# Kernel optimization log

Measured on AMD Instinct MI355X. Metric: run time of the kernel, lower is better.

Reference implementation:

```python
import jax, jax.numpy as jnp
import numpy as np

D_MODEL = 1024
NUM_HEADS = 16
DEPTH = D_MODEL // NUM_HEADS
B, S = 4, 2048


def setup_inputs() -> dict:
    key = jax.random.key(0)
    ks = jax.random.split(key, 11)
    sc = 1.0 / np.sqrt(D_MODEL)
    return {
        "query": jax.random.normal(ks[0], (B, S, D_MODEL), jnp.float32),
        "key_": jax.random.normal(ks[1], (B, S, D_MODEL), jnp.float32),
        "value": jax.random.normal(ks[2], (B, S, D_MODEL), jnp.float32),
        # torch Linear: y = x @ W.T + b, W shape [out, in]
        "Wq": jax.random.normal(ks[3], (D_MODEL, D_MODEL), jnp.float32) * sc,
        "bq": jax.random.normal(ks[4], (D_MODEL,), jnp.float32) * sc,
        "Wk": jax.random.normal(ks[5], (D_MODEL, D_MODEL), jnp.float32) * sc,
        "bk": jax.random.normal(ks[6], (D_MODEL,), jnp.float32) * sc,
        "Wv": jax.random.normal(ks[7], (D_MODEL, D_MODEL), jnp.float32) * sc,
        "bv": jax.random.normal(ks[8], (D_MODEL,), jnp.float32) * sc,
        "Wo": jax.random.normal(ks[9], (D_MODEL, D_MODEL), jnp.float32) * sc,
        "bo": jax.random.normal(ks[10], (D_MODEL,), jnp.float32) * sc,
    }


def _split_heads(x):
    # [B,S,D] -> [B,H,S,depth]
    b, s, _ = x.shape
    return x.reshape(b, s, NUM_HEADS, DEPTH).transpose(0, 2, 1, 3)


def reference(query, key_, value, Wq, bq, Wk, bk, Wv, bv, Wo, bo):
    Q = _split_heads(query @ Wq.T + bq)
    K = _split_heads(key_ @ Wk.T + bk)
    V = _split_heads(value @ Wv.T + bv)
    scale = 1.0 / jnp.sqrt(jnp.float32(DEPTH))
    scores = jnp.einsum("bhqd,bhkd->bhqk", Q, K) * scale  # [B,H,S,S]
    attention_weights = jax.nn.softmax(scores, axis=-1)
    out = jnp.einsum("bhqk,bhkd->bhqd", attention_weights, V)
    out = out.transpose(0, 2, 1, 3).reshape(query.shape[0], -1, D_MODEL)
    out = out @ Wo.T + bo
    return out, attention_weights
```

## Files before the change

kernel.cpp:

```cpp
#include <hip/hip_runtime.h>

#define NHEAD 16
#define SEQ 2048
#define DMODEL 1024
#define BB 4
#define MROWS (BB*SEQ)
#define NBH (BB*NHEAD)
#define NT (SEQ/32)

typedef float f32x4 __attribute__((ext_vector_type(4)));
typedef _Float16 f16x8 __attribute__((ext_vector_type(8)));
typedef _Float16 f16x4 __attribute__((ext_vector_type(4)));

static __device__ __forceinline__ f32x4 mfma16(f16x8 a, f16x8 b, f32x4 c) {
  return __builtin_amdgcn_mfma_f32_16x16x32_f16(a, b, c, 0, 0, 0);
}

static __device__ __forceinline__ void split2(float x, unsigned short& hi, unsigned short& lo) {
  _Float16 h = (_Float16)x;
  hi = __builtin_bit_cast(unsigned short, h);
  lo = __builtin_bit_cast(unsigned short, (_Float16)(x - (float)h));
}

static __device__ __forceinline__ void gload_lds16(const unsigned short* g, unsigned short* l) {
  __builtin_amdgcn_global_load_lds(
      (const __attribute__((address_space(1))) unsigned int*)g,
      (__attribute__((address_space(3))) unsigned int*)l, 16, 0, 0);
}

__global__ __launch_bounds__(256)
void round_f16(const float* __restrict__ src, unsigned short* __restrict__ dst, int n4)
{
  int i = blockIdx.x*256 + threadIdx.x;
  const int stride = gridDim.x*256;
  for (; i < n4; i += stride) {
    const float4 x = ((const float4*)src)[i];
    ushort4 h;
    h.x = __builtin_bit_cast(unsigned short, (_Float16)x.x);
    h.y = __builtin_bit_cast(unsigned short, (_Float16)x.y);
    h.z = __builtin_bit_cast(unsigned short, (_Float16)x.z);
    h.w = __builtin_bit_cast(unsigned short, (_Float16)x.w);
    ((ushort4*)dst)[i] = h;
  }
}

__global__ __launch_bounds__(256)
void split_f32(const float* __restrict__ src, unsigned short* __restrict__ hi,
               unsigned short* __restrict__ lo, int n4)
{
  int i = blockIdx.x*256 + threadIdx.x;
  const int stride = gridDim.x*256;
  for (; i < n4; i += stride) {
    const float4 x = ((const float4*)src)[i];
    ushort4 h, l;
    split2(x.x, h.x, l.x); split2(x.y, h.y, l.y);
    split2(x.z, h.z, l.z); split2(x.w, h.w, l.w);
    ((ushort4*)hi)[i] = h;
    ((ushort4*)lo)[i] = l;
  }
}

static __device__ __forceinline__ void stage_proj(
    unsigned short* ab, unsigned short* bb,
    const unsigned short* __restrict__ Xf,
    const unsigned short* __restrict__ Wh, const unsigned short* __restrict__ Wl,
    int m0, int n0, int k0, int tid)
{
#pragma unroll
  for (int r = 0; r < 2; ++r) {
    const int gi = r*256 + tid;
    const int row = gi >> 2, c = gi & 3;
    const int lg = c ^ ((row >> 1) & 3);
    gload_lds16(Xf + (size_t)(m0+row)*DMODEL + k0 + lg*8,
                ab + r*2048 + (tid & 0xC0)*8);
  }
#pragma unroll
  for (int r = 0; r < 4; ++r) {
    const int gi = r*256 + tid;
    const int row = gi >> 3, c = gi & 7;
    const int sg = c ^ (row & 7);
    const unsigned short* src = (sg < 4)
        ? (Wh + (size_t)(n0+row)*DMODEL + k0 + sg*8)
        : (Wl + (size_t)(n0+row)*DMODEL + k0 + (sg-4)*8);
    gload_lds16(src, bb + r*2048 + (tid & 0xC0)*8);
  }
}

template<int MODE>
__global__ __launch_bounds__(256, 3)
void proj_gemm(const unsigned short* __restrict__ Xf,
               const unsigned short* __restrict__ Wh, const unsigned short* __restrict__ Wl,
               const float* __restrict__ bias, float oscale,
               unsigned short* __restrict__ o16, float* __restrict__ o_f32)
{
  __shared__ unsigned short As[2][128][32];
  __shared__ unsigned short Bs[2][128][64];
  const int tid  = threadIdx.x;
  const int wid  = tid >> 6, lane = tid & 63;
  const int g    = lane >> 4, r16 = lane & 15;
  const int id   = blockIdx.y*64 + blockIdx.x;
  const int xcd  = id & 7, slot = id >> 3;
  const int m0   = (xcd*8 + (slot & 7)) * 128;
  const int n0   = (slot >> 3) * 128;
  const int wr   = wid >> 1, wc = wid & 1;

  f32x4 acc[4][4] = {};

  stage_proj(&As[0][0][0], &Bs[0][0][0], Xf, Wh, Wl, m0, n0, 0, tid);
  asm volatile("s_waitcnt vmcnt(0)" ::: "memory");
  __builtin_amdgcn_s_barrier();

  for (int kt = 0; kt < 32; ++kt) {
    const int cur = kt & 1;
    if (kt < 31)
      stage_proj(&As[cur^1][0][0], &Bs[cur^1][0][0], Xf, Wh, Wl, m0, n0, (kt+1)*32, tid);

    const unsigned short (*Asb)[32] = As[cur];
    const unsigned short (*Bsb)[64] = Bs[cur];
    f16x8 a[4], b_h[4], b_l[4];
#pragma unroll
    for (int t = 0; t < 4; ++t) {
      const int ar = wr*64 + t*16 + r16;
      a[t] = *(const f16x8*)((const char*)&Asb[ar][0] + ((g ^ ((ar >> 1) & 3)) << 4));
      const int br = wc*64 + t*16 + r16;
      const char* pb = (const char*)&Bsb[br][0];
      b_h[t] = *(const f16x8*)(pb + (((g    ) ^ (br & 7)) << 4));
      b_l[t] = *(const f16x8*)(pb + (((4 | g) ^ (br & 7)) << 4));
    }
    __builtin_amdgcn_s_setprio(1);
#pragma unroll
    for (int mt = 0; mt < 4; ++mt)
#pragma unroll
      for (int nt = 0; nt < 4; ++nt) {
        acc[mt][nt] = mfma16(a[mt], b_h[nt], acc[mt][nt]);
        acc[mt][nt] = mfma16(a[mt], b_l[nt], acc[mt][nt]);
      }
    __builtin_amdgcn_s_setprio(0);

    if (kt < 31) {
      asm volatile("s_waitcnt vmcnt(0)" ::: "memory");
      __builtin_amdgcn_s_barrier();
    }
  }

#pragma unroll
  for (int nt = 0; nt < 4; ++nt) {
    const int n  = n0 + wc*64 + nt*16 + r16;
    const float bn = bias[n];
#pragma unroll
    for (int mt = 0; mt < 4; ++mt) {
      const int mb = m0 + wr*64 + mt*16 + g*4;
      if (MODE == 0) {
#pragma unroll
        for (int j = 0; j < 4; ++j) {
          const int m = mb + j;
          const int bt = m >> 11, s = m & (SEQ-1);
          const int hh = n >> 6,  d = n & 63;
          o16[(((size_t)(bt*NHEAD + hh)*SEQ + s) << 6) + d] =
              __builtin_bit_cast(unsigned short, (_Float16)((acc[mt][nt][j] + bn) * oscale));
        }
      } else if (MODE == 1) {
        const int bt = mb >> 11, sb = mb & (SEQ-1);
        const int hh = n >> 6,  d = n & 63;
        ushort4 v;
        v.x = __builtin_bit_cast(unsigned short, (_Float16)(acc[mt][nt][0] + bn));
        v.y = __builtin_bit_cast(unsigned short, (_Float16)(acc[mt][nt][1] + bn));
        v.z = __builtin_bit_cast(unsigned short, (_Float16)(acc[mt][nt][2] + bn));
        v.w = __builtin_bit_cast(unsigned short, (_Float16)(acc[mt][nt][3] + bn));
        *(ushort4*)(o16 + ((size_t)(bt*NHEAD + hh)*64 + d)*SEQ + sb) = v;
      } else {
#pragma unroll
        for (int j = 0; j < 4; ++j)
          o_f32[(size_t)(mb + j)*DMODEL + n] = acc[mt][nt][j] + bn;
      }
    }
  }
}

static __device__ __forceinline__ void stage_k(unsigned short* dst,
    const unsigned short* __restrict__ Kf, size_t kbase, int k0, int tid)
{
  const int row = tid >> 3, c = tid & 7;
  const int sg = c ^ (row & 7);
  gload_lds16(Kf + kbase + (size_t)(k0+row)*64 + sg*8, dst + (tid & 0xC0)*8);
}

static __device__ __forceinline__ void stage_v(unsigned short* dst,
    const unsigned short* __restrict__ Vtg, int bh, int k0, int tid)
{
  const int row = tid >> 2, c = tid & 3;
  const int lg = c ^ ((row >> 1) & 3);
  gload_lds16(Vtg + ((size_t)bh*64 + row)*SEQ + k0 + lg*8, dst + (tid & 0xC0)*8);
}

__global__ __launch_bounds__(256, 4)
void attn_fused(const unsigned short* __restrict__ Qf, const unsigned short* __restrict__ Kf,
                const unsigned short* __restrict__ Vtg,
                float* __restrict__ wout, unsigned short* __restrict__ of16)
{
  __shared__ unsigned short Ks[4][32][64];
  __shared__ unsigned short Vs[4][64][32];
  __shared__ unsigned short PA[4][16][40];
  const int tid = threadIdx.x, wid = tid >> 6, lane = tid & 63;
  const int g = lane >> 4, r16 = lane & 15;
  const int id = blockIdx.y*32 + blockIdx.x;
  const int xcd = id & 7, slot = id >> 3;
  const int bh = (slot >> 5)*8 + xcd;
  const int bx = slot & 31;
  const int bt = bh >> 4, hh = bh & (NHEAD-1);
  const int s0 = bx*64 + wid*16;
  const size_t kbase = (size_t)bh*SEQ*64;

  const size_t qoff = ((size_t)bh*SEQ + s0 + r16)*64 + (size_t)g*8;
  const f16x8 qh0 = *(const f16x8*)(Qf + qoff);
  const f16x8 qh1 = *(const f16x8*)(Qf + qoff + 32);

  float lp = 0.f;
  stage_k(&Ks[0][0][0], Kf, kbase, 0, tid);
  stage_k(&Ks[1][0][0], Kf, kbase, 32, tid);
  asm volatile("s_waitcnt vmcnt(1)" ::: "memory");
  __builtin_amdgcn_s_barrier();
  for (int kt = 0; kt < NT; ++kt) {
    const int cur = kt & 3;
    const bool pf = kt < NT-2;
    if (pf) stage_k(&Ks[(kt+2)&3][0][0], Kf, kbase, (kt+2)*32, tid);
#pragma unroll
    for (int sub = 0; sub < 2; ++sub) {
      const int krow = sub*16 + r16;
      const char* pk = (const char*)&Ks[cur][krow][0];
      const int sx = krow & 7;
      const f16x8 kh0 = *(const f16x8*)(pk + (((g    ) ^ sx) << 4));
      const f16x8 kh1 = *(const f16x8*)(pk + (((4 | g) ^ sx) << 4));
      f32x4 acc = {};
      __builtin_amdgcn_s_setprio(1);
      acc = mfma16(kh0, qh0, acc);
      acc = mfma16(kh1, qh1, acc);
      __builtin_amdgcn_s_setprio(0);
#pragma unroll
      for (int j = 0; j < 4; ++j) lp += __builtin_exp2f(acc[j]);
    }
    if (pf) { asm volatile("s_waitcnt vmcnt(1)" ::: "memory"); }
    else    { asm volatile("s_waitcnt vmcnt(0)" ::: "memory"); }
    __builtin_amdgcn_s_barrier();
  }
  lp += __shfl_xor(lp, 16);
  lp += __shfl_xor(lp, 32);
  const float li = 1.0f / lp;

  f32x4 acco[4] = {};
  char* paw = (char*)&PA[wid][0][0];

  stage_k(&Ks[0][0][0], Kf, kbase, 0, tid);
  stage_v(&Vs[0][0][0], Vtg, bh, 0, tid);
  stage_k(&Ks[1][0][0], Kf, kbase, 32, tid);
  stage_v(&Vs[1][0][0], Vtg, bh, 32, tid);
  asm volatile("s_waitcnt vmcnt(2)" ::: "memory");
  __builtin_amdgcn_s_barrier();
  for (int kt = 0; kt < NT; ++kt) {
    const int cur = kt & 3;
    if (kt < NT-2) {
      stage_k(&Ks[(kt+2)&3][0][0], Kf, kbase, (kt+2)*32, tid);
      stage_v(&Vs[(kt+2)&3][0][0], Vtg, bh, (kt+2)*32, tid);
    }
#pragma unroll
    for (int sub = 0; sub < 2; ++sub) {
      const int krow = sub*16 + r16;
      const char* pk = (const char*)&Ks[cur][krow][0];
      const int sx = krow & 7;
      const f16x8 kh0 = *(const f16x8*)(pk + (((g    ) ^ sx) << 4));
      const f16x8 kh1 = *(const f16x8*)(pk + (((4 | g) ^ sx) << 4));
      f32x4 acc = {};
      __builtin_amdgcn_s_setprio(1);
      acc = mfma16(kh0, qh0, acc);
      acc = mfma16(kh1, qh1, acc);
      __builtin_amdgcn_s_setprio(0);
      f32x4 w4;
      f16x4 p4;
#pragma unroll
      for (int j = 0; j < 4; ++j) {
        w4[j] = __builtin_exp2f(acc[j]) * li;
        p4[j] = (_Float16)w4[j];
      }
      float* wp = wout + ((size_t)bh*SEQ + s0 + r16)*SEQ + kt*32 + sub*16 + 4*g;
      __builtin_nontemporal_store(w4, (f32x4*)wp);
      *(f16x4*)(paw + r16*80 + ((((2*sub + (g >> 1)) ^ (r16 & 3)) << 4) | ((g & 1) << 3))) = p4;
    }
    asm volatile("s_waitcnt lgkmcnt(0)" ::: "memory");
    const f16x8 pa = *(const f16x8*)(paw + r16*80 + ((g ^ (r16 & 3)) << 4));
    __builtin_amdgcn_s_setprio(1);
#pragma unroll
    for (int nt = 0; nt < 4; ++nt) {
      const int vrow = nt*16 + r16;
      const f16x8 vv = *(const f16x8*)((const char*)&Vs[cur][vrow][0] +
                                       ((g ^ ((vrow >> 1) & 3)) << 4));
      acco[nt] = mfma16(pa, vv, acco[nt]);
    }
    __builtin_amdgcn_s_setprio(0);
    if (kt == 0) {
      asm volatile("s_waitcnt vmcnt(4)" ::: "memory"); __builtin_amdgcn_s_barrier();
    } else if (kt < NT-2) {
      asm volatile("s_waitcnt vmcnt(6)" ::: "memory"); __builtin_amdgcn_s_barrier();
    } else if (kt == NT-2) {
      asm volatile("s_waitcnt vmcnt(4)" ::: "memory"); __builtin_amdgcn_s_barrier();
    }
  }

#pragma unroll
  for (int nt = 0; nt < 4; ++nt)
#pragma unroll
    for (int j = 0; j < 4; ++j)
      of16[((size_t)bt*SEQ + s0 + 4*g + j)*DMODEL + hh*64 + nt*16 + r16] =
          __builtin_bit_cast(unsigned short, (_Float16)acco[nt][j]);
}

extern "C" void kernel_launch(void* const* d_in, const int* in_sizes, int n_in,
                              void* d_out, int out_size, void* d_ws, size_t ws_size,
                              hipStream_t stream)
{
  const float* query = (const float*)d_in[0];
  const float* key_  = (const float*)d_in[1];
  const float* value = (const float*)d_in[2];
  const float* Wq = (const float*)d_in[3];
  const float* bq = (const float*)d_in[4];
  const float* Wk = (const float*)d_in[5];
  const float* bk = (const float*)d_in[6];
  const float* Wv = (const float*)d_in[7];
  const float* bv = (const float*)d_in[8];
  const float* Wo = (const float*)d_in[9];
  const float* bo = (const float*)d_in[10];

  const size_t NE = (size_t)NBH * SEQ * 64;
  unsigned short* X16 = (unsigned short*)d_ws;
  unsigned short* Qf  = X16 + NE;
  unsigned short* Kf  = Qf + NE;
  unsigned short* Vt  = Kf + NE;
  unsigned short* Of  = Vt + NE;
  unsigned short* WH  = Of + NE;
  unsigned short* WL  = WH + (size_t)DMODEL*DMODEL;

  float* out0  = (float*)d_out;
  float* wattn = out0 + (size_t)MROWS * DMODEL;

  const int nX4 = MROWS*DMODEL/4, nW4 = DMODEL*DMODEL/4;
  const float QSCALE = 0.125f * 1.4426950408889634f;
  dim3 gg(64, 8);

  round_f16<<<1024, 256, 0, stream>>>(query, X16, nX4);
  split_f32<<<512,  256, 0, stream>>>(Wq, WH, WL, nW4);
  proj_gemm<0><<<gg, dim3(256), 0, stream>>>(X16, WH, WL, bq, QSCALE, Qf, nullptr);

  round_f16<<<1024, 256, 0, stream>>>(key_, X16, nX4);
  split_f32<<<512,  256, 0, stream>>>(Wk, WH, WL, nW4);
  proj_gemm<0><<<gg, dim3(256), 0, stream>>>(X16, WH, WL, bk, 1.0f, Kf, nullptr);

  round_f16<<<1024, 256, 0, stream>>>(value, X16, nX4);
  split_f32<<<512,  256, 0, stream>>>(Wv, WH, WL, nW4);
  proj_gemm<1><<<gg, dim3(256), 0, stream>>>(X16, WH, WL, bv, 1.0f, Vt, nullptr);

  attn_fused<<<dim3(32, NBH), dim3(256), 0, stream>>>(Qf, Kf, Vt, wattn, Of);

  split_f32<<<512,  256, 0, stream>>>(Wo, WH, WL, nW4);
  proj_gemm<2><<<gg, dim3(256), 0, stream>>>(Of, WH, WL, bo, 1.0f, nullptr, out0);
}
```

Baseline: 558.3 us.

## Drop fp16 hi/lo weight split, use single fp16 weights in projections

Weights are now rounded to a single fp16 copy instead of a hi/lo fp16 pair, which halves the MFMA count and the B-tile LDS/global traffic in every projection GEMM. The per-tensor conversion kernels are batched into one launch for the three activations and one launch for the four weights, with separate workspace buffers for each. Launch bounds change from 3 to 2 waves per SIMD. The cost is lower weight precision, since the residual correction term is gone, which may push the output error closer to tolerance.

```diff
diff --git a/kernel.cpp b/kernel.cpp
--- a/kernel.cpp
+++ b/kernel.cpp
@@ -16,54 +16,54 @@
   return __builtin_amdgcn_mfma_f32_16x16x32_f16(a, b, c, 0, 0, 0);
 }
 
-static __device__ __forceinline__ void split2(float x, unsigned short& hi, unsigned short& lo) {
-  _Float16 h = (_Float16)x;
-  hi = __builtin_bit_cast(unsigned short, h);
-  lo = __builtin_bit_cast(unsigned short, (_Float16)(x - (float)h));
-}
-
 static __device__ __forceinline__ void gload_lds16(const unsigned short* g, unsigned short* l) {
   __builtin_amdgcn_global_load_lds(
       (const __attribute__((address_space(1))) unsigned int*)g,
       (__attribute__((address_space(3))) unsigned int*)l, 16, 0, 0);
 }
 
+static __device__ __forceinline__ ushort4 cvt4(float4 x) {
+  ushort4 h;
+  h.x = __builtin_bit_cast(unsigned short, (_Float16)x.x);
+  h.y = __builtin_bit_cast(unsigned short, (_Float16)x.y);
+  h.z = __builtin_bit_cast(unsigned short, (_Float16)x.z);
+  h.w = __builtin_bit_cast(unsigned short, (_Float16)x.w);
+  return h;
+}
+
 __global__ __launch_bounds__(256)
-void round_f16(const float* __restrict__ src, unsigned short* __restrict__ dst, int n4)
-{
+void round3_f16(const float* __restrict__ q, const float* __restrict__ k,
+                const float* __restrict__ v,
+                unsigned short* __restrict__ oq, unsigned short* __restrict__ ok,
+                unsigned short* __restrict__ ov, int n4)
+{
+  const float* src = (blockIdx.y == 0) ? q : (blockIdx.y == 1) ? k : v;
+  unsigned short* dst = (blockIdx.y == 0) ? oq : (blockIdx.y == 1) ? ok : ov;
   int i = blockIdx.x*256 + threadIdx.x;
   const int stride = gridDim.x*256;
-  for (; i < n4; i += stride) {
-    const float4 x = ((const float4*)src)[i];
-    ushort4 h;
-    h.x = __builtin_bit_cast(unsigned short, (_Float16)x.x);
-    h.y = __builtin_bit_cast(unsigned short, (_Float16)x.y);
-    h.z = __builtin_bit_cast(unsigned short, (_Float16)x.z);
-    h.w = __builtin_bit_cast(unsigned short, (_Float16)x.w);
-    ((ushort4*)dst)[i] = h;
-  }
+  for (; i < n4; i += stride)
+    ((ushort4*)dst)[i] = cvt4(((const float4*)src)[i]);
 }
 
 __global__ __launch_bounds__(256)
-void split_f32(const float* __restrict__ src, unsigned short* __restrict__ hi,
-               unsigned short* __restrict__ lo, int n4)
-{
+void round_w4(const float* __restrict__ w0, const float* __restrict__ w1,
+              const float* __restrict__ w2, const float* __restrict__ w3,
+              unsigned short* __restrict__ o0, unsigned short* __restrict__ o1,
+              unsigned short* __restrict__ o2, unsigned short* __restrict__ o3, int n4)
+{
+  const float* src = (blockIdx.y == 0) ? w0 : (blockIdx.y == 1) ? w1
+                   : (blockIdx.y == 2) ? w2 : w3;
+  unsigned short* dst = (blockIdx.y == 0) ? o0 : (blockIdx.y == 1) ? o1
+                      : (blockIdx.y == 2) ? o2 : o3;
   int i = blockIdx.x*256 + threadIdx.x;
   const int stride = gridDim.x*256;
-  for (; i < n4; i += stride) {
-    const float4 x = ((const float4*)src)[i];
-    ushort4 h, l;
-    split2(x.x, h.x, l.x); split2(x.y, h.y, l.y);
-    split2(x.z, h.z, l.z); split2(x.w, h.w, l.w);
-    ((ushort4*)hi)[i] = h;
-    ((ushort4*)lo)[i] = l;
-  }
+  for (; i < n4; i += stride)
+    ((ushort4*)dst)[i] = cvt4(((const float4*)src)[i]);
 }
 
 static __device__ __forceinline__ void stage_proj(
     unsigned short* ab, unsigned short* bb,
-    const unsigned short* __restrict__ Xf,
-    const unsigned short* __restrict__ Wh, const unsigned short* __restrict__ Wl,
+    const unsigned short* __restrict__ Xf, const unsigned short* __restrict__ Wf,
     int m0, int n0, int k0, int tid)
 {
 #pragma unroll
@@ -75,26 +75,23 @@
                 ab + r*2048 + (tid & 0xC0)*8);
   }
 #pragma unroll
-  for (int r = 0; r < 4; ++r) {
+  for (int r = 0; r < 2; ++r) {
     const int gi = r*256 + tid;
-    const int row = gi >> 3, c = gi & 7;
-    const int sg = c ^ (row & 7);
-    const unsigned short* src = (sg < 4)
-        ? (Wh + (size_t)(n0+row)*DMODEL + k0 + sg*8)
-        : (Wl + (size_t)(n0+row)*DMODEL + k0 + (sg-4)*8);
-    gload_lds16(src, bb + r*2048 + (tid & 0xC0)*8);
+    const int row = gi >> 2, c = gi & 3;
+    const int lg = c ^ ((row >> 1) & 3);
+    gload_lds16(Wf + (size_t)(n0+row)*DMODEL + k0 + lg*8,
+                bb + r*2048 + (tid & 0xC0)*8);
   }
 }
 
 template<int MODE>
-__global__ __launch_bounds__(256, 3)
-void proj_gemm(const unsigned short* __restrict__ Xf,
-               const unsigned short* __restrict__ Wh, const unsigned short* __restrict__ Wl,
+__global__ __launch_bounds__(256, 2)
+void proj_gemm(const unsigned short* __restrict__ Xf, const unsigned short* __restrict__ Wf,
                const float* __restrict__ bias, float oscale,
                unsigned short* __restrict__ o16, float* __restrict__ o_f32)
 {
   __shared__ unsigned short As[2][128][32];
-  __shared__ unsigned short Bs[2][128][64];
+  __shared__ unsigned short Bs[2][128][32];
   const int tid  = threadIdx.x;
   const int wid  = tid >> 6, lane = tid & 63;
   const int g    = lane >> 4, r16 = lane & 15;
@@ -106,35 +103,31 @@
 
   f32x4 acc[4][4] = {};
 
-  stage_proj(&As[0][0][0], &Bs[0][0][0], Xf, Wh, Wl, m0, n0, 0, tid);
+  stage_proj(&As[0][0][0], &Bs[0][0][0], Xf, Wf, m0, n0, 0, tid);
   asm volatile("s_waitcnt vmcnt(0)" ::: "memory");
   __builtin_amdgcn_s_barrier();
 
   for (int kt = 0; kt < 32; ++kt) {
     const int cur = kt & 1;
     if (kt < 31)
-      stage_proj(&As[cur^1][0][0], &Bs[cur^1][0][0], Xf, Wh, Wl, m0, n0, (kt+1)*32, tid);
+      stage_proj(&As[cur^1][0][0], &Bs[cur^1][0][0], Xf, Wf, m0, n0, (kt+1)*32, tid);
 
     const unsigned short (*Asb)[32] = As[cur];
-    const unsigned short (*Bsb)[64] = Bs[cur];
-    f16x8 a[4], b_h[4], b_l[4];
+    const unsigned short (*Bsb)[32] = Bs[cur];
+    f16x8 a[4], b[4];
 #pragma unroll
     for (int t = 0; t < 4; ++t) {
       const int ar = wr*64 + t*16 + r16;
       a[t] = *(const f16x8*)((const char*)&Asb[ar][0] + ((g ^ ((ar >> 1) & 3)) << 4));
       const int br = wc*64 + t*16 + r16;
-      const char* pb = (const char*)&Bsb[br][0];
-      b_h[t] = *(const f16x8*)(pb + (((g    ) ^ (br & 7)) << 4));
-      b_l[t] = *(const f16x8*)(pb + (((4 | g) ^ (br & 7)) << 4));
+      b[t] = *(const f16x8*)((const char*)&Bsb[br][0] + ((g ^ ((br >> 1) & 3)) << 4));
     }
     __builtin_amdgcn_s_setprio(1);
 #pragma unroll
     for (int mt = 0; mt < 4; ++mt)
 #pragma unroll
-      for (int nt = 0; nt < 4; ++nt) {
-        acc[mt][nt] = mfma16(a[mt], b_h[nt], acc[mt][nt]);
-        acc[mt][nt] = mfma16(a[mt], b_l[nt], acc[mt][nt]);
-      }
+      for (int nt = 0; nt < 4; ++nt)
+        acc[mt][nt] = mfma16(a[mt], b[nt], acc[mt][nt]);
     __builtin_amdgcn_s_setprio(0);
 
     if (kt < 31) {
@@ -330,13 +323,18 @@
   const float* bo = (const float*)d_in[10];
 
   const size_t NE = (size_t)NBH * SEQ * 64;
-  unsigned short* X16 = (unsigned short*)d_ws;
-  unsigned short* Qf  = X16 + NE;
-  unsigned short* Kf  = Qf + NE;
-  unsigned short* Vt  = Kf + NE;
-  unsigned short* Of  = Vt + NE;
-  unsigned short* WH  = Of + NE;
-  unsigned short* WL  = WH + (size_t)DMODEL*DMODEL;
+  const size_t NW = (size_t)DMODEL * DMODEL;
+  unsigned short* Xq16 = (unsigned short*)d_ws;
+  unsigned short* Xk16 = Xq16 + NE;
+  unsigned short* Xv16 = Xk16 + NE;
+  unsigned short* Qf   = Xv16 + NE;
+  unsigned short* Kf   = Qf + NE;
+  unsigned short* Vt   = Kf + NE;
+  unsigned short* Wq16 = Vt + NE;
+  unsigned short* Wk16 = Wq16 + NW;
+  unsigned short* Wv16 = Wk16 + NW;
+  unsigned short* Wo16 = Wv16 + NW;
+  unsigned short* Of   = Xq16;
 
   float* out0  = (float*)d_out;
   float* wattn = out0 + (size_t)MROWS * DMODEL;
@@ -345,20 +343,14 @@
   const float QSCALE = 0.125f * 1.4426950408889634f;
   dim3 gg(64, 8);
 
-  round_f16<<<1024, 256, 0, stream>>>(query, X16, nX4);
-  split_f32<<<512,  256, 0, stream>>>(Wq, WH, WL, nW4);
-  proj_gemm<0><<<gg, dim3(256), 0, stream>>>(X16, WH, WL, bq, QSCALE, Qf, nullptr);
-
-  round_f16<<<1024, 256, 0, stream>>>(key_, X16, nX4);
-  split_f32<<<512,  256, 0, stream>>>(Wk, WH, WL, nW4);
-  proj_gemm<0><<<gg, dim3(256), 0, stream>>>(X16, WH, WL, bk, 1.0f, Kf, nullptr);
-
-  round_f16<<<1024, 256, 0, stream>>>(value, X16, nX4);
-  split_f32<<<512,  256, 0, stream>>>(Wv, WH, WL, nW4);
-  proj_gemm<1><<<gg, dim3(256), 0, stream>>>(X16, WH, WL, bv, 1.0f, Vt, nullptr);
+  round3_f16<<<dim3(1024, 3), 256, 0, stream>>>(query, key_, value, Xq16, Xk16, Xv16, nX4);
+  round_w4<<<dim3(256, 4), 256, 0, stream>>>(Wq, Wk, Wv, Wo, Wq16, Wk16, Wv16, Wo16, nW4);
+
+  proj_gemm<0><<<gg, dim3(256), 0, stream>>>(Xq16, Wq16, bq, QSCALE, Qf, nullptr);
+  proj_gemm<0><<<gg, dim3(256), 0, stream>>>(Xk16, Wk16, bk, 1.0f, Kf, nullptr);
+  proj_gemm<1><<<gg, dim3(256), 0, stream>>>(Xv16, Wv16, bv, 1.0f, Vt, nullptr);
 
   attn_fused<<<dim3(32, NBH), dim3(256), 0, stream>>>(Qf, Kf, Vt, wattn, Of);
 
-  split_f32<<<512,  256, 0, stream>>>(Wo, WH, WL, nW4);
-  proj_gemm<2><<<gg, dim3(256), 0, stream>>>(Of, WH, WL, bo, 1.0f, nullptr, out0);
-}
+  proj_gemm<2><<<gg, dim3(256), 0, stream>>>(Of, Wo16, bo, 1.0f, nullptr, out0);
+}
```

Measured after the change: 497.7 us (median of 2 runs). -10.9%, faster.
